# Optimization experiments

Measured on AMD Instinct MI355X. Metric: run time of the kernel, lower is better.

Reference implementation:

```python
import jax, jax.numpy as jnp
import numpy as np

H = W = 56
WS = 7          # window size
SHIFT = 3       # shift size
HEADS = 4
DIM = 128
NUM_MLP = 512
EPS = 1e-5


def _build_rel_index():
    ch = np.arange(WS)
    cw = np.arange(WS)
    coords = np.stack(np.meshgrid(ch, cw, indexing='ij')).reshape(2, -1)  # [2,49]
    rel = coords[:, :, None] - coords[:, None, :]                         # [2,49,49]
    rel = rel.transpose(1, 2, 0)
    rel[:, :, 0] += WS - 1
    rel[:, :, 1] += WS - 1
    rel[:, :, 0] *= 2 * WS - 1
    return rel.sum(-1).astype(np.int32)                                   # [49,49]


def _build_attn_mask():
    mask = np.zeros((H, W), dtype=np.float32)
    slices = (slice(0, -WS), slice(-WS, -SHIFT), slice(-SHIFT, None))
    cnt = 0
    for hs in slices:
        for ws_ in slices:
            mask[hs, ws_] = cnt
            cnt += 1
    nH, nW = H // WS, W // WS
    mw = mask.reshape(nH, WS, nW, WS).transpose(0, 2, 1, 3).reshape(nH * nW, WS * WS)
    am = mw[:, None, :] - mw[:, :, None]
    return np.where(am != 0, -100.0, 0.0).astype(np.float32)              # [64,49,49]


def setup_inputs() -> dict:
    key = jax.random.key(0)
    ks = jax.random.split(key, 8)
    B = 64
    s = 0.02
    return {
        'x': jax.random.normal(ks[0], (B, H * W, DIM), jnp.float32),
        'ln1_g': jnp.ones((DIM,), jnp.float32),
        'ln1_b': jnp.zeros((DIM,), jnp.float32),
        'eca_w': jax.random.normal(ks[1], (3, DIM, 1), jnp.float32) * s,
        'qkv_w': jax.random.normal(ks[2], (DIM, 3 * DIM), jnp.float32) * s,
        'qkv_b': jnp.zeros((3 * DIM,), jnp.float32),
        'rel_bias_table': jax.random.normal(ks[3], ((2 * WS - 1) ** 2, HEADS), jnp.float32) * s,
        'proj_w': jax.random.normal(ks[4], (DIM, DIM), jnp.float32) * s,
        'proj_b': jnp.zeros((DIM,), jnp.float32),
        'ln2_g': jnp.ones((DIM,), jnp.float32),
        'ln2_b': jnp.zeros((DIM,), jnp.float32),
        'mlp_w1': jax.random.normal(ks[5], (DIM, NUM_MLP), jnp.float32) * s,
        'mlp_b1': jnp.zeros((NUM_MLP,), jnp.float32),
        'mlp_w2': jax.random.normal(ks[6], (NUM_MLP, DIM), jnp.float32) * s,
        'mlp_b2': jnp.zeros((DIM,), jnp.float32),
        'attn_mask': jnp.asarray(_build_attn_mask()),
        'rel_index': jnp.asarray(_build_rel_index()),
    }


def _layer_norm(x, g, b):
    mu = x.mean(-1, keepdims=True)
    var = jnp.mean((x - mu) ** 2, -1, keepdims=True)
    return (x - mu) * jax.lax.rsqrt(var + EPS) * g + b


def _forward(x, ln1_g, ln1_b, eca_w, qkv_w, qkv_b, rel_bias_table, proj_w, proj_b,
             ln2_g, ln2_b, mlp_w1, mlp_b1, mlp_w2, mlp_b2, attn_mask, rel_index):
    B, L, C = x.shape
    nH, nW = H // WS, W // WS
    nwin = nH * nW
    hd = C // HEADS
    scale = hd ** -0.5

    x_skip = x
    xs = _layer_norm(x, ln1_g, ln1_b)
    x4 = xs.reshape(B, H, W, C)

    # Efficient channel attention (faithful: Conv1D over a length-1 steps axis,
    # 'same' padding -> only the center kernel tap contributes; gate is [B,1,1])
    sq = x4.mean((1, 2))[:, None, :]                                  # [B,1,C]
    gate = jax.lax.conv_general_dilated(
        sq, eca_w, (1,), 'SAME', dimension_numbers=('NWC', 'WIO', 'NWC'))  # [B,1,1]
    gate = jax.nn.sigmoid(gate)
    cattn = (x4 * gate[:, :, :, None]).reshape(B, H * W, C)

    # cyclic shift + window partition (batch-major, standard Swin layout)
    shifted = jnp.roll(x4, (-SHIFT, -SHIFT), (1, 2))
    xw = shifted.reshape(B, nH, WS, nW, WS, C).transpose(0, 1, 3, 2, 4, 5)
    xw = xw.reshape(B * nwin, WS * WS, C)                              # [Bn,49,C]

    # window attention with gathered relative position bias
    qkv = (xw @ qkv_w + qkv_b).reshape(-1, WS * WS, 3, HEADS, hd)
    qkv = qkv.transpose(2, 0, 3, 1, 4)                                 # [3,Bn,h,49,hd]
    q, k, v = qkv[0], qkv[1], qkv[2]
    attn = jnp.einsum('bhqd,bhkd->bhqk', q * scale, k)                 # [Bn,h,49,49]
    bias = rel_bias_table[rel_index.reshape(-1)]                       # [49*49,h]
    bias = bias.reshape(WS * WS, WS * WS, HEADS).transpose(2, 0, 1)    # [h,49,49]
    attn = attn + bias[None]
    attn = attn.reshape(B, nwin, HEADS, WS * WS, WS * WS) + attn_mask[None, :, None]
    attn = jax.nn.softmax(attn.reshape(-1, HEADS, WS * WS, WS * WS), -1)
    out = jnp.einsum('bhqk,bhkd->bqhd', attn, v).reshape(-1, WS * WS, C)
    out = out @ proj_w + proj_b                                        # [Bn,49,C]

    # window reverse + reverse shift
    out = out.reshape(B, nH, nW, WS, WS, C).transpose(0, 1, 3, 2, 4, 5)
    out = out.reshape(B, H, W, C)
    out = jnp.roll(out, (SHIFT, SHIFT), (1, 2)).reshape(B, H * W, C)

    x = x_skip + out + cattn
    x_skip = x
    xn = _layer_norm(x, ln2_g, ln2_b)
    h1 = jax.nn.gelu(xn @ mlp_w1 + mlp_b1, approximate=False)
    return x_skip + (h1 @ mlp_w2 + mlp_b2)


def reference(x, ln1_g, ln1_b, eca_w, qkv_w, qkv_b, rel_bias_table, proj_w, proj_b,
              ln2_g, ln2_b, mlp_w1, mlp_b1, mlp_w2, mlp_b2, attn_mask, rel_index):
    return _forward(x, ln1_g, ln1_b, eca_w, qkv_w, qkv_b, rel_bias_table, proj_w,
                    proj_b, ln2_g, ln2_b, mlp_w1, mlp_b1, mlp_w2, mlp_b2,
                    attn_mask, rel_index)
```

## Files before the change

kernel.cpp:

```cpp
#include <hip/hip_runtime.h>
#include <hip/hip_bf16.h>
#include <math.h>

#define B_    64
#define Himg  56
#define Wimg  56
#define L_    (Himg*Wimg)
#define WS_   7
#define SHIFT 3
#define NWIN  64
#define NTOK  49
#define HEADS 4
#define HD    32
#define DIM   128
#define NMLP  512
#define EPS   1e-5f
#define SCALE 0.17677669529663687f

typedef __hip_bfloat16 bf16;
typedef __attribute__((ext_vector_type(8))) short short8;
typedef __attribute__((ext_vector_type(4))) float floatx4;
typedef __attribute__((ext_vector_type(4))) unsigned short ushort4v;
#define MFMA16(a, b, c) __builtin_amdgcn_mfma_f32_16x16x32_bf16(a, b, c, 0, 0, 0)

__device__ float g_gacc[B_];
__device__ __align__(16) unsigned short g_w1t[NMLP * DIM];
__device__ __align__(16) unsigned short g_w2t[DIM * NMLP];
__device__ __align__(16) unsigned short g_qkvwt[3 * DIM * DIM];
__device__ __align__(16) unsigned short g_pwt[DIM * DIM];
__device__ float g_combo[NWIN * HEADS * NTOK * NTOK];

__device__ __forceinline__ float us2f(unsigned short u) {
  return __uint_as_float(((unsigned int)u) << 16);
}
__device__ __forceinline__ unsigned short f2us(float f) {
  unsigned int x = __float_as_uint(f);
  x += 0x7fffu + ((x >> 16) & 1u);
  return (unsigned short)(x >> 16);
}
__device__ __forceinline__ bool is_bf(const void* ones) {
  return ((const unsigned int*)ones)[0] == 0x3F803F80u;
}
template<bool BF>
__device__ __forceinline__ float ldf(const void* p, size_t i) {
  if (BF) return __bfloat162float(((const bf16*)p)[i]);
  return ((const float*)p)[i];
}
template<bool BF>
__device__ __forceinline__ floatx4 ld4(const void* p, size_t i) {
  if (BF) {
    const ushort4v u = *(const ushort4v*)((const unsigned short*)p + i);
    floatx4 r = {us2f(u.x), us2f(u.y), us2f(u.z), us2f(u.w)};
    return r;
  }
  return *(const floatx4*)((const float*)p + i);
}
template<bool BF>
__device__ __forceinline__ void st4(void* p, size_t i, floatx4 v) {
  if (BF) {
    ushort4v u = {f2us(v.x), f2us(v.y), f2us(v.z), f2us(v.w)};
    *(ushort4v*)((unsigned short*)p + i) = u;
  } else {
    *(floatx4*)((float*)p + i) = v;
  }
}
__device__ __forceinline__ float gelu_t(float x) {
  float y = 0.7978845608028654f * (x + 0.044715f * x * x * x);
  y = fminf(fmaxf(y, -15.f), 15.f);
  const float e = __expf(2.f * y);
  return 0.5f * x * (1.f + (e - 1.f) / (e + 1.f));
}

template<bool BF>
__global__ void k_prep(const void* __restrict__ w1, const void* __restrict__ w2,
                       const void* __restrict__ qkvw, const void* __restrict__ pw,
                       const void* __restrict__ rbt, const void* __restrict__ amask,
                       const int* __restrict__ ridx, const void* __restrict__ ones) {
  if (is_bf(ones) != BF) return;
  const int bid = blockIdx.x, tid = threadIdx.x;
  if (bid == 0 && tid < B_) g_gacc[tid] = 0.f;
  if (bid < 256) {
    const int idx = bid * 256 + tid;
    { const int k = idx >> 9, n = idx & 511; g_w1t[n * DIM + k] = f2us(ldf<BF>(w1, idx)); }
    { const int k = idx >> 7, n = idx & 127; g_w2t[n * NMLP + k] = f2us(ldf<BF>(w2, idx)); }
  } else if (bid < 448) {
    const int idx = (bid - 256) * 256 + tid;
    { const int k = idx / 384, n = idx % 384; g_qkvwt[n * DIM + k] = f2us(ldf<BF>(qkvw, idx)); }
    if (idx < DIM * DIM) {
      const int k = idx >> 7, n = idx & 127;
      g_pwt[n * DIM + k] = f2us(ldf<BF>(pw, idx));
    }
  } else {
    const int wh_ = bid - 448;
    const int widx = wh_ >> 2, h = wh_ & 3;
    for (int idx = tid; idx < NTOK * NTOK; idx += 256) {
      g_combo[(size_t)wh_ * (NTOK * NTOK) + idx] =
          ldf<BF>(rbt, (size_t)ridx[idx] * HEADS + h) +
          ldf<BF>(amask, (size_t)widx * (NTOK * NTOK) + idx);
    }
  }
}

template<bool BF>
__global__ void k_gate_partial(const void* __restrict__ x,
                               const void* __restrict__ ln1_g,
                               const void* __restrict__ ln1_b,
                               const void* __restrict__ eca_w) {
  if (is_bf(ln1_g) != BF) return;
  const int b = blockIdx.x;
  const int lane = threadIdx.x & 63;
  const int wave = threadIdx.x >> 6;
  const int c4 = (lane & 31) * 4;
  const floatx4 g4  = ld4<BF>(ln1_g, c4);
  const floatx4 be4 = ld4<BF>(ln1_b, c4);
  const floatx4 w4  = ld4<BF>(eca_w, DIM + c4);
  float acc = 0.f;
  const int t0 = blockIdx.y * 8 + wave * 2 + (lane >> 5);
  for (int t = t0; t < L_; t += 256) {
    const floatx4 v = ld4<BF>(x, ((size_t)b * L_ + t) * DIM + c4);
    float s = v.x + v.y + v.z + v.w;
    float s2 = v.x * v.x + v.y * v.y + v.z * v.z + v.w * v.w;
    #pragma unroll
    for (int m = 1; m <= 16; m <<= 1) {
      s  += __shfl_xor(s,  m, 64);
      s2 += __shfl_xor(s2, m, 64);
    }
    const float mu = s * (1.f / DIM);
    const float rs = rsqrtf(s2 * (1.f / DIM) - mu * mu + EPS);
    acc += ((v.x - mu) * rs * g4.x + be4.x) * w4.x
         + ((v.y - mu) * rs * g4.y + be4.y) * w4.y
         + ((v.z - mu) * rs * g4.z + be4.z) * w4.z
         + ((v.w - mu) * rs * g4.w + be4.w) * w4.w;
  }
  #pragma unroll
  for (int m = 1; m <= 32; m <<= 1) acc += __shfl_xor(acc, m, 64);
  if (lane == 0) atomicAdd(&g_gacc[b], acc);
}

template<bool BF>
__global__ __launch_bounds__(512, 4) void k_attn_mfma(
    const void* __restrict__ x,
    const void* __restrict__ ln1_g, const void* __restrict__ ln1_b,
    const void* __restrict__ qkv_b, const void* __restrict__ proj_b,
    void* __restrict__ x2) {
  if (is_bf(ln1_g) != BF) return;
  __shared__ __align__(16) unsigned short q_s[NTOK * 136];
  __shared__ __align__(16) unsigned short k_s[NTOK * 136];
  __shared__ __align__(16) unsigned short xno[NTOK * 136];
  __shared__ __align__(16) unsigned short vt[128 * 72];
  __shared__ __align__(16) unsigned short Pb[8 * 16 * 40];
  __shared__ float mu[NTOK], rs[NTOK];
  __shared__ int off_s[NTOK];
  unsigned short* o_s = q_s;

  const int tid = threadIdx.x;
  const int bw = blockIdx.x;
  const int b = bw >> 6, widx = bw & 63;
  const int wh = widx >> 3, wc = widx & 7;
  const int w = tid >> 6, l = tid & 63;
  const int pair = w >> 1, p = w & 1;
  const int lr = l & 15, lq = l >> 4;

  {
    const int i = tid >> 3, j = tid & 7;
    if (i < NTOK) {
      const int r = i / 7, qq = i % 7;
      const int oh = (wh * 7 + r + SHIFT) % Himg;
      const int ow = (wc * 7 + qq + SHIFT) % Wimg;
      const int sp = oh * Wimg + ow;
      if (j == 0) off_s[i] = sp;
      const size_t base = ((size_t)b * L_ + sp) * DIM;
      const int c0 = j * 16;
      const floatx4 v0 = ld4<BF>(x, base + c0);
      const floatx4 v1 = ld4<BF>(x, base + c0 + 4);
      const floatx4 v2 = ld4<BF>(x, base + c0 + 8);
      const floatx4 v3 = ld4<BF>(x, base + c0 + 12);
      float s = v0.x + v0.y + v0.z + v0.w + v1.x + v1.y + v1.z + v1.w
              + v2.x + v2.y + v2.z + v2.w + v3.x + v3.y + v3.z + v3.w;
      float s2 = v0.x * v0.x + v0.y * v0.y + v0.z * v0.z + v0.w * v0.w
               + v1.x * v1.x + v1.y * v1.y + v1.z * v1.z + v1.w * v1.w
               + v2.x * v2.x + v2.y * v2.y + v2.z * v2.z + v2.w * v2.w
               + v3.x * v3.x + v3.y * v3.y + v3.z * v3.z + v3.w * v3.w;
      s  += __shfl_xor(s, 1, 64);  s  += __shfl_xor(s, 2, 64);  s  += __shfl_xor(s, 4, 64);
      s2 += __shfl_xor(s2, 1, 64); s2 += __shfl_xor(s2, 2, 64); s2 += __shfl_xor(s2, 4, 64);
      const float m = s * (1.f / DIM);
      const float rr = rsqrtf(s2 * (1.f / DIM) - m * m + EPS);
      if (j == 0) { mu[i] = m; rs[i] = rr; }
      const floatx4 g0 = ld4<BF>(ln1_g, c0),     g1 = ld4<BF>(ln1_g, c0 + 4);
      const floatx4 g2 = ld4<BF>(ln1_g, c0 + 8), g3 = ld4<BF>(ln1_g, c0 + 12);
      const floatx4 e0 = ld4<BF>(ln1_b, c0),     e1 = ld4<BF>(ln1_b, c0 + 4);
      const floatx4 e2 = ld4<BF>(ln1_b, c0 + 8), e3 = ld4<BF>(ln1_b, c0 + 12);
      short8 o0, o1;
      o0[0] = (short)f2us((v0.x - m) * rr * g0.x + e0.x);
      o0[1] = (short)f2us((v0.y - m) * rr * g0.y + e0.y);
      o0[2] = (short)f2us((v0.z - m) * rr * g0.z + e0.z);
      o0[3] = (short)f2us((v0.w - m) * rr * g0.w + e0.w);
      o0[4] = (short)f2us((v1.x - m) * rr * g1.x + e1.x);
      o0[5] = (short)f2us((v1.y - m) * rr * g1.y + e1.y);
      o0[6] = (short)f2us((v1.z - m) * rr * g1.z + e1.z);
      o0[7] = (short)f2us((v1.w - m) * rr * g1.w + e1.w);
      o1[0] = (short)f2us((v2.x - m) * rr * g2.x + e2.x);
      o1[1] = (short)f2us((v2.y - m) * rr * g2.y + e2.y);
      o1[2] = (short)f2us((v2.z - m) * rr * g2.z + e2.z);
      o1[3] = (short)f2us((v2.w - m) * rr * g2.w + e2.w);
      o1[4] = (short)f2us((v3.x - m) * rr * g3.x + e3.x);
      o1[5] = (short)f2us((v3.y - m) * rr * g3.y + e3.y);
      o1[6] = (short)f2us((v3.z - m) * rr * g3.z + e3.z);
      o1[7] = (short)f2us((v3.w - m) * rr * g3.w + e3.w);
      *(short8*)&xno[i * 136 + c0] = o0;
      *(short8*)&xno[i * 136 + c0 + 8] = o1;
    } else {
      const short8 zz = {0, 0, 0, 0, 0, 0, 0, 0};
      for (int z = tid - NTOK * 8; z < 256; z += 512 - NTOK * 8) {
        const int d = z >> 1, o = (z & 1) * 8;
        *(short8*)&vt[d * 72 + 48 + o] = zz;
      }
    }
  }
  __syncthreads();

  {
    const int mp = p;
    for (int np = 0; np < 3; np++) {
      const int n0 = pair * 96 + np * 32 + lr;
      const int n1 = n0 + 16;
      floatx4 a00 = {0.f, 0.f, 0.f, 0.f}, a01 = a00, a10 = a00, a11 = a00;
      #pragma unroll
      for (int kc = 0; kc < 4; kc++) {
        const int k0 = kc * 32 + lq * 8;
        const short8 A0 = *(const short8*)&xno[(mp * 32 + lr) * 136 + k0];
        const short8 A1 = *(const short8*)&xno[(mp * 32 + 16 + lr) * 136 + k0];
        const short8 B0 = *(const short8*)&g_qkvwt[n0 * DIM + k0];
        const short8 B1 = *(const short8*)&g_qkvwt[n1 * DIM + k0];
        a00 = MFMA16(A0, B0, a00); a01 = MFMA16(A0, B1, a01);
        a10 = MFMA16(A1, B0, a10); a11 = MFMA16(A1, B1, a11);
      }
      const float bb0 = ldf<BF>(qkv_b, n0), bb1 = ldf<BF>(qkv_b, n1);
      #pragma unroll
      for (int r = 0; r < 4; r++) {
        const int i0 = mp * 32 + lq * 4 + r, i1 = i0 + 16;
        #pragma unroll
        for (int t = 0; t < 4; t++) {
          const int i = (t & 2) ? i1 : i0;
          const int n = (t & 1) ? n1 : n0;
          const float val = (t == 0 ? a00[r] : t == 1 ? a01[r] : t == 2 ? a10[r] : a11[r])
                            + ((t & 1) ? bb1 : bb0);
          if (i < NTOK) {
            const unsigned short hv = f2us(val);
            if (n < DIM) q_s[i * 136 + n] = hv;
            else if (n < 2 * DIM) k_s[i * 136 + (n - DIM)] = hv;
            else vt[(n - 2 * DIM) * 72 + i] = hv;
          }
        }
      }
    }
  }
  __syncthreads();

  {
    const int h = pair;
    unsigned short* Pw = &Pb[w * 16 * 40];
    const size_t cbase = (size_t)((widx << 2) + h) * (NTOK * NTOK);
    for (int mm = 0; mm < 2; mm++) {
      const int mi = p * 2 + mm;
      const short8 Aq = *(const short8*)&q_s[(mi * 16 + lr) * 136 + h * 32 + lq * 8];
      float sv[4][4];
      #pragma unroll
      for (int ni = 0; ni < 4; ni++) {
        const short8 Bk = *(const short8*)&k_s[(ni * 16 + lr) * 136 + h * 32 + lq * 8];
        floatx4 z = {0.f, 0.f, 0.f, 0.f};
        const floatx4 sc = MFMA16(Aq, Bk, z);
        const int j = ni * 16 + lr;
        #pragma unroll
        for (int r = 0; r < 4; r++) {
          const int i = mi * 16 + lq * 4 + r;
          float s = -1e30f;
          if (i < NTOK && j < NTOK)
            s = sc[r] * SCALE + g_combo[cbase + i * NTOK + j];
          sv[ni][r] = s;
        }
      }
      float inv[4];
      #pragma unroll
      for (int r = 0; r < 4; r++) {
        float m = fmaxf(fmaxf(sv[0][r], sv[1][r]), fmaxf(sv[2][r], sv[3][r]));
        m = fmaxf(m, __shfl_xor(m, 1, 64)); m = fmaxf(m, __shfl_xor(m, 2, 64));
        m = fmaxf(m, __shfl_xor(m, 4, 64)); m = fmaxf(m, __shfl_xor(m, 8, 64));
        float s = 0.f;
        #pragma unroll
        for (int ni = 0; ni < 4; ni++) { sv[ni][r] = __expf(sv[ni][r] - m); s += sv[ni][r]; }
        s += __shfl_xor(s, 1, 64); s += __shfl_xor(s, 2, 64);
        s += __shfl_xor(s, 4, 64); s += __shfl_xor(s, 8, 64);
        inv[r] = 1.f / s;
      }
      floatx4 o0 = {0.f, 0.f, 0.f, 0.f}, o1 = o0;
      #pragma unroll
      for (int kq = 0; kq < 2; kq++) {
        #pragma unroll
        for (int nn = 0; nn < 2; nn++) {
          const int ni = kq * 2 + nn;
          #pragma unroll
          for (int r = 0; r < 4; r++)
            Pw[(lq * 4 + r) * 40 + nn * 16 + lr] = f2us(sv[ni][r] * inv[r]);
        }
        const short8 Ap  = *(const short8*)&Pw[lr * 40 + lq * 8];
        const short8 Bv0 = *(const short8*)&vt[(h * 32 + lr) * 72 + kq * 32 + lq * 8];
        const short8 Bv1 = *(const short8*)&vt[(h * 32 + 16 + lr) * 72 + kq * 32 + lq * 8];
        o0 = MFMA16(Ap, Bv0, o0);
        o1 = MFMA16(Ap, Bv1, o1);
      }
      #pragma unroll
      for (int r = 0; r < 4; r++) {
        const int i = mi * 16 + lq * 4 + r;
        if (i < NTOK) {
          xno[i * 136 + h * 32 + lr]      = f2us(o0[r]);
          xno[i * 136 + h * 32 + 16 + lr] = f2us(o1[r]);
        }
      }
    }
  }
  __syncthreads();

  {
    const int mp = p;
    const int n0 = pair * 32 + lr, n1 = n0 + 16;
    floatx4 a00 = {0.f, 0.f, 0.f, 0.f}, a01 = a00, a10 = a00, a11 = a00;
    #pragma unroll
    for (int kc = 0; kc < 4; kc++) {
      const int k0 = kc * 32 + lq * 8;
      const short8 A0 = *(const short8*)&xno[(mp * 32 + lr) * 136 + k0];
      const short8 A1 = *(const short8*)&xno[(mp * 32 + 16 + lr) * 136 + k0];
      const short8 B0 = *(const short8*)&g_pwt[n0 * DIM + k0];
      const short8 B1 = *(const short8*)&g_pwt[n1 * DIM + k0];
      a00 = MFMA16(A0, B0, a00); a01 = MFMA16(A0, B1, a01);
      a10 = MFMA16(A1, B0, a10); a11 = MFMA16(A1, B1, a11);
    }
    const float pb0 = ldf<BF>(proj_b, n0), pb1 = ldf<BF>(proj_b, n1);
    #pragma unroll
    for (int r = 0; r < 4; r++) {
      const int i0 = mp * 32 + lq * 4 + r, i1 = i0 + 16;
      if (i0 < NTOK) {
        o_s[i0 * 136 + n0] = f2us(a00[r] + pb0);
        o_s[i0 * 136 + n1] = f2us(a01[r] + pb1);
      }
      if (i1 < NTOK) {
        o_s[i1 * 136 + n0] = f2us(a10[r] + pb0);
        o_s[i1 * 136 + n1] = f2us(a11[r] + pb1);
      }
    }
  }
  __syncthreads();
  {
    const float gb = 1.f / (1.f + __expf(-g_gacc[b] * (1.f / (float)L_)));
    for (int idx = tid; idx < NTOK * 32; idx += 512) {
      const int i = idx >> 5, c4 = (idx & 31) * 4;
      const size_t pos = ((size_t)b * L_ + off_s[i]) * DIM + c4;
      const floatx4 xv = ld4<BF>(x, pos);
      const ushort4v o4 = *(const ushort4v*)&o_s[i * 136 + c4];
      const floatx4 g4 = ld4<BF>(ln1_g, c4);
      const floatx4 b4 = ld4<BF>(ln1_b, c4);
      const float m = mu[i], rr = rs[i];
      floatx4 out;
      out.x = xv.x + us2f(o4.x) + gb * ((xv.x - m) * rr * g4.x + b4.x);
      out.y = xv.y + us2f(o4.y) + gb * ((xv.y - m) * rr * g4.y + b4.y);
      out.z = xv.z + us2f(o4.z) + gb * ((xv.z - m) * rr * g4.z + b4.z);
      out.w = xv.w + us2f(o4.w) + gb * ((xv.w - m) * rr * g4.w + b4.w);
      st4<BF>(x2, pos, out);
    }
  }
}

template<bool BF>
__global__ __launch_bounds__(512, 6) void k_mlp_mfma(
    const void* __restrict__ ln2_g, const void* __restrict__ ln2_b,
    const void* __restrict__ b1v, const void* __restrict__ b2v,
    void* __restrict__ io) {
  if (is_bf(ln2_g) != BF) return;
  __shared__ __align__(16) unsigned short xn[64][136];
  __shared__ __align__(16) unsigned short h1[64][264];
  const int tid = threadIdx.x;
  const size_t t0 = (size_t)blockIdx.x * 64;
  const int w = tid >> 6, l = tid & 63;
  const int lr = l & 15, lq = l >> 4;

  {
    const int i = tid >> 3, c0 = (tid & 7) * 16;
    const size_t base = (t0 + i) * DIM + c0;
    const floatx4 va = ld4<BF>(io, base);
    const floatx4 vb = ld4<BF>(io, base + 4);
    const floatx4 vc = ld4<BF>(io, base + 8);
    const floatx4 vd = ld4<BF>(io, base + 12);
    float s = va.x + va.y + va.z + va.w + vb.x + vb.y + vb.z + vb.w
            + vc.x + vc.y + vc.z + vc.w + vd.x + vd.y + vd.z + vd.w;
    float s2 = va.x * va.x + va.y * va.y + va.z * va.z + va.w * va.w
             + vb.x * vb.x + vb.y * vb.y + vb.z * vb.z + vb.w * vb.w
             + vc.x * vc.x + vc.y * vc.y + vc.z * vc.z + vc.w * vc.w
             + vd.x * vd.x + vd.y * vd.y + vd.z * vd.z + vd.w * vd.w;
    s  += __shfl_xor(s, 1, 64);  s  += __shfl_xor(s, 2, 64);  s  += __shfl_xor(s, 4, 64);
    s2 += __shfl_xor(s2, 1, 64); s2 += __shfl_xor(s2, 2, 64); s2 += __shfl_xor(s2, 4, 64);
    const float m = s * (1.f / DIM);
    const float rr = rsqrtf(s2 * (1.f / DIM) - m * m + EPS);
    const floatx4 g0 = ld4<BF>(ln2_g, c0),     g1 = ld4<BF>(ln2_g, c0 + 4);
    const floatx4 g2 = ld4<BF>(ln2_g, c0 + 8), g3 = ld4<BF>(ln2_g, c0 + 12);
    const floatx4 e0 = ld4<BF>(ln2_b, c0),     e1 = ld4<BF>(ln2_b, c0 + 4);
    const floatx4 e2 = ld4<BF>(ln2_b, c0 + 8), e3 = ld4<BF>(ln2_b, c0 + 12);
    short8 o0, o1;
    o0[0] = (short)f2us((va.x - m) * rr * g0.x + e0.x);
    o0[1] = (short)f2us((va.y - m) * rr * g0.y + e0.y);
    o0[2] = (short)f2us((va.z - m) * rr * g0.z + e0.z);
    o0[3] = (short)f2us((va.w - m) * rr * g0.w + e0.w);
    o0[4] = (short)f2us((vb.x - m) * rr * g1.x + e1.x);
    o0[5] = (short)f2us((vb.y - m) * rr * g1.y + e1.y);
    o0[6] = (short)f2us((vb.z - m) * rr * g1.z + e1.z);
    o0[7] = (short)f2us((vb.w - m) * rr * g1.w + e1.w);
    o1[0] = (short)f2us((vc.x - m) * rr * g2.x + e2.x);
    o1[1] = (short)f2us((vc.y - m) * rr * g2.y + e2.y);
    o1[2] = (short)f2us((vc.z - m) * rr * g2.z + e2.z);
    o1[3] = (short)f2us((vc.w - m) * rr * g2.w + e2.w);
    o1[4] = (short)f2us((vd.x - m) * rr * g3.x + e3.x);
    o1[5] = (short)f2us((vd.y - m) * rr * g3.y + e3.y);
    o1[6] = (short)f2us((vd.z - m) * rr * g3.z + e3.z);
    o1[7] = (short)f2us((vd.w - m) * rr * g3.w + e3.w);
    *(short8*)&xn[i][c0] = o0;
    *(short8*)&xn[i][c0 + 8] = o1;
  }
  __syncthreads();

  floatx4 c2[4] = {{0.f, 0.f, 0.f, 0.f}, {0.f, 0.f, 0.f, 0.f},
                   {0.f, 0.f, 0.f, 0.f}, {0.f, 0.f, 0.f, 0.f}};

  #pragma unroll
  for (int half = 0; half < 2; half++) {
    {
      const int n0 = half * 256 + w * 32 + lr;
      const int n1 = n0 + 16;
      floatx4 a0[4] = {{0.f, 0.f, 0.f, 0.f}, {0.f, 0.f, 0.f, 0.f},
                       {0.f, 0.f, 0.f, 0.f}, {0.f, 0.f, 0.f, 0.f}};
      floatx4 a1[4] = {{0.f, 0.f, 0.f, 0.f}, {0.f, 0.f, 0.f, 0.f},
                       {0.f, 0.f, 0.f, 0.f}, {0.f, 0.f, 0.f, 0.f}};
      #pragma unroll
      for (int kc = 0; kc < 4; kc++) {
        const int k0 = kc * 32 + lq * 8;
        const short8 B0 = *(const short8*)&g_w1t[n0 * DIM + k0];
        const short8 B1 = *(const short8*)&g_w1t[n1 * DIM + k0];
        #pragma unroll
        for (int mt = 0; mt < 4; mt++) {
          const short8 A = *(const short8*)&xn[mt * 16 + lr][k0];
          a0[mt] = MFMA16(A, B0, a0[mt]);
          a1[mt] = MFMA16(A, B1, a1[mt]);
        }
      }
      const float bb0 = ldf<BF>(b1v, n0);
      const float bb1 = ldf<BF>(b1v, n1);
      const int hc0 = w * 32 + lr;
      #pragma unroll
      for (int mt = 0; mt < 4; mt++) {
        #pragma unroll
        for (int r = 0; r < 4; r++) {
          const int row = mt * 16 + lq * 4 + r;
          h1[row][hc0]      = f2us(gelu_t(a0[mt][r] + bb0));
          h1[row][hc0 + 16] = f2us(gelu_t(a1[mt][r] + bb1));
        }
      }
    }
    __syncthreads();

    {
      const int nc = w * 16 + lr;
      const int kb = half * 256;
      #pragma unroll
      for (int kc = 0; kc < 8; kc++) {
        const int k0 = kc * 32 + lq * 8;
        const short8 B = *(const short8*)&g_w2t[nc * NMLP + kb + k0];
        #pragma unroll
        for (int mt = 0; mt < 4; mt++) {
          const short8 A = *(const short8*)&h1[mt * 16 + lr][k0];
          c2[mt] = MFMA16(A, B, c2[mt]);
        }
      }
    }
    __syncthreads();
  }

  {
    const int nc = w * 16 + lr;
    const float bb = ldf<BF>(b2v, nc);
    #pragma unroll
    for (int mt = 0; mt < 4; mt++) {
      #pragma unroll
      for (int r = 0; r < 4; r++) {
        const int row = mt * 16 + lq * 4 + r;
        xn[row][nc] = f2us(c2[mt][r] + bb);
      }
    }
  }
  __syncthreads();

  for (int idx = tid; idx < 64 * 32; idx += 512) {
    const int i = idx >> 5, c4 = (idx & 31) * 4;
    const size_t pos = (t0 + i) * DIM + c4;
    const floatx4 v = ld4<BF>(io, pos);
    const ushort4v o4 = *(const ushort4v*)&xn[i][c4];
    floatx4 out = {v.x + us2f(o4.x), v.y + us2f(o4.y),
                   v.z + us2f(o4.z), v.w + us2f(o4.w)};
    st4<BF>(io, pos, out);
  }
}

extern "C" void kernel_launch(void* const* d_in, const int* in_sizes, int n_in,
                              void* d_out, int out_size, void* d_ws, size_t ws_size,
                              hipStream_t stream) {
  const void* x     = d_in[0];
  const void* ln1g  = d_in[1];
  const void* ln1b  = d_in[2];
  const void* ecaw  = d_in[3];
  const void* qkvw  = d_in[4];
  const void* qkvb  = d_in[5];
  const void* rbt   = d_in[6];
  const void* projw = d_in[7];
  const void* projb = d_in[8];
  const void* ln2g  = d_in[9];
  const void* ln2b  = d_in[10];
  const void* w1    = d_in[11];
  const void* b1    = d_in[12];
  const void* w2    = d_in[13];
  const void* b2    = d_in[14];
  const void* amask = d_in[15];
  const int*  ridx  = (const int*)d_in[16];

  const int gsz = in_sizes[1];
  const bool launch_bf = (gsz != 512);
  const bool launch_fp = (gsz != 256);

  if (launch_bf) k_prep<true ><<<704, 256, 0, stream>>>(w1, w2, qkvw, projw, rbt, amask, ridx, ln1g);
  if (launch_fp) k_prep<false><<<704, 256, 0, stream>>>(w1, w2, qkvw, projw, rbt, amask, ridx, ln1g);
  if (launch_bf) k_gate_partial<true ><<<dim3(B_, 32), 256, 0, stream>>>(x, ln1g, ln1b, ecaw);
  if (launch_fp) k_gate_partial<false><<<dim3(B_, 32), 256, 0, stream>>>(x, ln1g, ln1b, ecaw);
  if (launch_bf) k_attn_mfma<true ><<<B_ * NWIN, 512, 0, stream>>>(x, ln1g, ln1b, qkvb, projb, d_out);
  if (launch_fp) k_attn_mfma<false><<<B_ * NWIN, 512, 0, stream>>>(x, ln1g, ln1b, qkvb, projb, d_out);
  if (launch_bf) k_mlp_mfma<true ><<<(B_ * L_) / 64, 512, 0, stream>>>(ln2g, ln2b, b1, b2, d_out);
  if (launch_fp) k_mlp_mfma<false><<<(B_ * L_) / 64, 512, 0, stream>>>(ln2g, ln2b, b1, b2, d_out);
}
```

Before: 598.0 us.

## Compute transposed attention scores to keep softmax probabilities in registers

The attention step now computes S^T = K·Q^T, so each lane holds one query's scores across keys. The softmax reduction then needs only two cross-lane shuffles, and the probabilities are repacked into the PV MFMA B-operand with register shuffles instead of a round trip through shared memory. K and V fragments are hoisted out of the query loop, and the precomputed bias/mask table is stored transposed so its reads match the new layout. This removes the Pb shared buffer and its LDS traffic, at the cost of extra shuffle instructions and higher register pressure.

```diff
diff --git a/kernel.cpp b/kernel.cpp
--- a/kernel.cpp
+++ b/kernel.cpp
@@ -20,6 +20,7 @@
 typedef __hip_bfloat16 bf16;
 typedef __attribute__((ext_vector_type(8))) short short8;
 typedef __attribute__((ext_vector_type(4))) float floatx4;
+typedef __attribute__((ext_vector_type(4))) int intx4;
 typedef __attribute__((ext_vector_type(4))) unsigned short ushort4v;
 #define MFMA16(a, b, c) __builtin_amdgcn_mfma_f32_16x16x32_bf16(a, b, c, 0, 0, 0)
 
@@ -94,9 +95,10 @@
     const int wh_ = bid - 448;
     const int widx = wh_ >> 2, h = wh_ & 3;
     for (int idx = tid; idx < NTOK * NTOK; idx += 256) {
+      const int jj = idx / NTOK, ii = idx - jj * NTOK;
       g_combo[(size_t)wh_ * (NTOK * NTOK) + idx] =
-          ldf<BF>(rbt, (size_t)ridx[idx] * HEADS + h) +
-          ldf<BF>(amask, (size_t)widx * (NTOK * NTOK) + idx);
+          ldf<BF>(rbt, (size_t)ridx[ii * NTOK + jj] * HEADS + h) +
+          ldf<BF>(amask, (size_t)widx * (NTOK * NTOK) + ii * NTOK + jj);
     }
   }
 }
@@ -148,7 +150,6 @@
   __shared__ __align__(16) unsigned short k_s[NTOK * 136];
   __shared__ __align__(16) unsigned short xno[NTOK * 136];
   __shared__ __align__(16) unsigned short vt[128 * 72];
-  __shared__ __align__(16) unsigned short Pb[8 * 16 * 40];
   __shared__ float mu[NTOK], rs[NTOK];
   __shared__ int off_s[NTOK];
   unsigned short* o_s = q_s;
@@ -259,62 +260,90 @@
 
   {
     const int h = pair;
-    unsigned short* Pw = &Pb[w * 16 * 40];
     const size_t cbase = (size_t)((widx << 2) + h) * (NTOK * NTOK);
+    short8 Ak[4], Av[4];
+    #pragma unroll
+    for (int ni = 0; ni < 4; ni++)
+      Ak[ni] = *(const short8*)&k_s[(ni * 16 + lr) * 136 + h * 32 + lq * 8];
+    #pragma unroll
+    for (int half = 0; half < 2; half++)
+      #pragma unroll
+      for (int kq = 0; kq < 2; kq++)
+        Av[half * 2 + kq] =
+            *(const short8*)&vt[(h * 32 + half * 16 + lr) * 72 + kq * 32 + lq * 8];
+
+    const int s0lane = (l & 15) | ((l & 16) << 1);
+    const int s1lane = s0lane + 16;
+    const bool selhi = (l >> 5) & 1;
+
     for (int mm = 0; mm < 2; mm++) {
       const int mi = p * 2 + mm;
-      const short8 Aq = *(const short8*)&q_s[(mi * 16 + lr) * 136 + h * 32 + lq * 8];
+      const int iq = mi * 16 + lr;
+      const short8 Bq = *(const short8*)&q_s[iq * 136 + h * 32 + lq * 8];
       float sv[4][4];
       #pragma unroll
       for (int ni = 0; ni < 4; ni++) {
-        const short8 Bk = *(const short8*)&k_s[(ni * 16 + lr) * 136 + h * 32 + lq * 8];
         floatx4 z = {0.f, 0.f, 0.f, 0.f};
-        const floatx4 sc = MFMA16(Aq, Bk, z);
-        const int j = ni * 16 + lr;
+        const floatx4 sc = MFMA16(Ak[ni], Bq, z);
         #pragma unroll
         for (int r = 0; r < 4; r++) {
-          const int i = mi * 16 + lq * 4 + r;
+          const int j = ni * 16 + lq * 4 + r;
           float s = -1e30f;
-          if (i < NTOK && j < NTOK)
-            s = sc[r] * SCALE + g_combo[cbase + i * NTOK + j];
+          if (iq < NTOK && j < NTOK)
+            s = sc[r] * SCALE + g_combo[cbase + j * NTOK + iq];
           sv[ni][r] = s;
         }
       }
-      float inv[4];
-      #pragma unroll
-      for (int r = 0; r < 4; r++) {
-        float m = fmaxf(fmaxf(sv[0][r], sv[1][r]), fmaxf(sv[2][r], sv[3][r]));
-        m = fmaxf(m, __shfl_xor(m, 1, 64)); m = fmaxf(m, __shfl_xor(m, 2, 64));
-        m = fmaxf(m, __shfl_xor(m, 4, 64)); m = fmaxf(m, __shfl_xor(m, 8, 64));
-        float s = 0.f;
-        #pragma unroll
-        for (int ni = 0; ni < 4; ni++) { sv[ni][r] = __expf(sv[ni][r] - m); s += sv[ni][r]; }
-        s += __shfl_xor(s, 1, 64); s += __shfl_xor(s, 2, 64);
-        s += __shfl_xor(s, 4, 64); s += __shfl_xor(s, 8, 64);
-        inv[r] = 1.f / s;
-      }
-      floatx4 o0 = {0.f, 0.f, 0.f, 0.f}, o1 = o0;
+      float m0 = fmaxf(fmaxf(sv[0][0], sv[0][1]), fmaxf(sv[0][2], sv[0][3]));
+      float m1 = fmaxf(fmaxf(sv[1][0], sv[1][1]), fmaxf(sv[1][2], sv[1][3]));
+      float m2 = fmaxf(fmaxf(sv[2][0], sv[2][1]), fmaxf(sv[2][2], sv[2][3]));
+      float m3 = fmaxf(fmaxf(sv[3][0], sv[3][1]), fmaxf(sv[3][2], sv[3][3]));
+      float mx = fmaxf(fmaxf(m0, m1), fmaxf(m2, m3));
+      mx = fmaxf(mx, __shfl_xor(mx, 16, 64));
+      mx = fmaxf(mx, __shfl_xor(mx, 32, 64));
+      float ss = 0.f;
+      #pragma unroll
+      for (int ni = 0; ni < 4; ni++) {
+        #pragma unroll
+        for (int r = 0; r < 4; r++) { sv[ni][r] = __expf(sv[ni][r] - mx); }
+        ss += (sv[ni][0] + sv[ni][1]) + (sv[ni][2] + sv[ni][3]);
+      }
+      ss += __shfl_xor(ss, 16, 64);
+      ss += __shfl_xor(ss, 32, 64);
+      const float inv = 1.f / ss;
+      int pk_lo[4], pk_hi[4];
+      #pragma unroll
+      for (int ni = 0; ni < 4; ni++) {
+        pk_lo[ni] = (int)((unsigned)f2us(sv[ni][0] * inv) |
+                          ((unsigned)f2us(sv[ni][1] * inv) << 16));
+        pk_hi[ni] = (int)((unsigned)f2us(sv[ni][2] * inv) |
+                          ((unsigned)f2us(sv[ni][3] * inv) << 16));
+      }
+      floatx4 oc0 = {0.f, 0.f, 0.f, 0.f}, oc1 = oc0;
       #pragma unroll
       for (int kq = 0; kq < 2; kq++) {
-        #pragma unroll
-        for (int nn = 0; nn < 2; nn++) {
-          const int ni = kq * 2 + nn;
-          #pragma unroll
-          for (int r = 0; r < 4; r++)
-            Pw[(lq * 4 + r) * 40 + nn * 16 + lr] = f2us(sv[ni][r] * inv[r]);
-        }
-        const short8 Ap  = *(const short8*)&Pw[lr * 40 + lq * 8];
-        const short8 Bv0 = *(const short8*)&vt[(h * 32 + lr) * 72 + kq * 32 + lq * 8];
-        const short8 Bv1 = *(const short8*)&vt[(h * 32 + 16 + lr) * 72 + kq * 32 + lq * 8];
-        o0 = MFMA16(Ap, Bv0, o0);
-        o1 = MFMA16(Ap, Bv1, o1);
-      }
-      #pragma unroll
-      for (int r = 0; r < 4; r++) {
-        const int i = mi * 16 + lq * 4 + r;
-        if (i < NTOK) {
-          xno[i * 136 + h * 32 + lr]      = f2us(o0[r]);
-          xno[i * 136 + h * 32 + 16 + lr] = f2us(o1[r]);
+        const int a_lo0 = __shfl(pk_lo[2 * kq],     s0lane, 64);
+        const int a_lo1 = __shfl(pk_lo[2 * kq + 1], s0lane, 64);
+        const int a_hi0 = __shfl(pk_hi[2 * kq],     s0lane, 64);
+        const int a_hi1 = __shfl(pk_hi[2 * kq + 1], s0lane, 64);
+        const int b_lo0 = __shfl(pk_lo[2 * kq],     s1lane, 64);
+        const int b_lo1 = __shfl(pk_lo[2 * kq + 1], s1lane, 64);
+        const int b_hi0 = __shfl(pk_hi[2 * kq],     s1lane, 64);
+        const int b_hi1 = __shfl(pk_hi[2 * kq + 1], s1lane, 64);
+        intx4 t;
+        t.x = selhi ? a_lo1 : a_lo0;
+        t.y = selhi ? a_hi1 : a_hi0;
+        t.z = selhi ? b_lo1 : b_lo0;
+        t.w = selhi ? b_hi1 : b_hi0;
+        const short8 Bp = *(const short8*)&t;
+        oc0 = MFMA16(Av[kq], Bp, oc0);
+        oc1 = MFMA16(Av[2 + kq], Bp, oc1);
+      }
+      if (iq < NTOK) {
+        #pragma unroll
+        for (int r = 0; r < 4; r++) {
+          xno[iq * 136 + h * 32 + lq * 4 + r]      = f2us(oc0[r]);
+          xno[iq * 136 + h * 32 + 16 + lq * 4 + r] = f2us(oc1[r]);
         }
       }
     }
```

After: 594.5 us. Within noise of the previous version (-0.6%).
